# Kernel tuning notes

Hardware: AMD Instinct MI355X
Metric: run time of the kernel (lower is better)

## Reference

```python
import jax, jax.numpy as jnp
import numpy as np

N = 50000
E = 800000
F_IN = 500
H = 5          # heads
C = 32         # per-head channels
HID = H * C    # 160
NC = 20        # num_classes
G = 8          # number of graphs in batch
SLOPE_ATT = 0.2   # GATConv attention leaky slope (PyG default)
SLOPE_ACT = 0.01  # F.leaky_relu default


def _layernorm(x, scale, bias, eps=1e-5):
    mu = jnp.mean(x, axis=-1, keepdims=True)
    var = jnp.var(x, axis=-1, keepdims=True)
    return (x - mu) * jax.lax.rsqrt(var + eps) * scale + bias


def _edge_softmax(logits, dst, num_nodes):
    # segment softmax over incoming edges of each destination node
    m = jax.ops.segment_max(logits, dst, num_segments=num_nodes)
    ex = jnp.exp(logits - m[dst])
    s = jax.ops.segment_sum(ex, dst, num_segments=num_nodes)
    return ex / (s[dst] + 1e-16)


def _gat_layer(x, src, dst, W, a_src, a_dst, b):
    n = x.shape[0]
    h = (x @ W).reshape(n, H, C)                       # [N,H,C]
    al_s = jnp.einsum('nhc,hc->nh', h, a_src)          # [N,H]
    al_d = jnp.einsum('nhc,hc->nh', h, a_dst)
    logits = jax.nn.leaky_relu(al_s[src] + al_d[dst], SLOPE_ATT)  # [Et,H]
    alpha = _edge_softmax(logits, dst, n)              # [Et,H]
    msg = h[src] * alpha[..., None]                    # [Et,H,C]
    out = jax.ops.segment_sum(msg, dst, num_segments=n).reshape(n, HID) + b
    return out, alpha


def setup_inputs():
    key = jax.random.key(0)
    ks = jax.random.split(key, 24)
    p = lambda k, shp: jax.random.normal(k, shp, jnp.float32) * 0.05
    x = jax.random.normal(ks[0], (N, F_IN), jnp.float32)
    edge_index = jax.random.randint(ks[1], (2, E), 0, N, jnp.int64)
    batch = jnp.sort(jax.random.randint(ks[2], (N,), 0, G, jnp.int64))
    return {
        'x': x, 'edge_index': edge_index, 'batch': batch,
        'W1': p(ks[3], (F_IN, HID)), 'a_src1': p(ks[4], (H, C)), 'a_dst1': p(ks[5], (H, C)), 'b1': jnp.zeros((HID,), jnp.float32),
        'ln1_s': jnp.ones((HID,), jnp.float32), 'ln1_b': jnp.zeros((HID,), jnp.float32),
        'W2': p(ks[6], (HID, HID)), 'a_src2': p(ks[7], (H, C)), 'a_dst2': p(ks[8], (H, C)), 'b2': jnp.zeros((HID,), jnp.float32),
        'ln2_s': jnp.ones((HID,), jnp.float32), 'ln2_b': jnp.zeros((HID,), jnp.float32),
        'Wm': p(ks[9], (HID, HID)), 'bm': jnp.zeros((HID,), jnp.float32),
        'Wmlp1': p(ks[10], (HID, HID)), 'bmlp1': jnp.zeros((HID,), jnp.float32),
        'ln3_s': jnp.ones((HID,), jnp.float32), 'ln3_b': jnp.zeros((HID,), jnp.float32),
        'Wmlp2': p(ks[11], (HID, NC)), 'bmlp2': jnp.zeros((NC,), jnp.float32),
    }


def reference(x, edge_index, batch, W1, a_src1, a_dst1, b1, ln1_s, ln1_b,
              W2, a_src2, a_dst2, b2, ln2_s, ln2_b, Wm, bm,
              Wmlp1, bmlp1, ln3_s, ln3_b, Wmlp2, bmlp2):
    n = x.shape[0]
    # PyG GATConv adds self-loops by default
    loops = jnp.arange(n, dtype=edge_index.dtype)
    src = jnp.concatenate([edge_index[0], loops])
    dst = jnp.concatenate([edge_index[1], loops])

    h1, alpha1 = _gat_layer(x, src, dst, W1, a_src1, a_dst1, b1)
    h1 = jax.nn.leaky_relu(h1, SLOPE_ACT)
    h1 = _layernorm(h1, ln1_s, ln1_b)      # dropout = identity at eval

    h2, alpha2 = _gat_layer(h1, src, dst, W2, a_src2, a_dst2, b2)
    h2 = jax.nn.leaky_relu(h2, SLOPE_ACT)
    h2 = _layernorm(h2, ln2_s, ln2_b)

    xo = jax.nn.leaky_relu(h2 @ Wm + bm, SLOPE_ACT)   # [N,HID]

    # global_mean_pool over batch assignment
    sums = jax.ops.segment_sum(xo, batch, num_segments=G)
    cnts = jax.ops.segment_sum(jnp.ones((n, 1), xo.dtype), batch, num_segments=G)
    pooled = sums / jnp.maximum(cnts, 1.0)            # [G,HID]

    z = pooled @ Wmlp1 + bmlp1
    z = jax.nn.relu(_layernorm(z, ln3_s, ln3_b))
    rec = z @ Wmlp2 + bmlp2                           # [G,NC]
    return xo, rec, alpha1, alpha2
```

## Files before the change

kernel.cpp:

```cpp
#include <hip/hip_runtime.h>
#include <hip/hip_bf16.h>
#include <cstdint>
#include <cstddef>

#define NN   50000
#define EE   800000
#define ET_  (EE + NN)
#define FIN  500
#define HID_ 160
#define NC_  20
#define GG   8
#define GB1  ((NN + 63) / 64)
#define NK1  16
#define NK2  5
#define EBH  ((ET_ + 255) / 256)

typedef __attribute__((ext_vector_type(8))) short ab8;
typedef __attribute__((ext_vector_type(4))) float f4;

static __device__ __forceinline__ unsigned short f2bf(float v) {
    union { float f; uint32_t u; } c; c.f = v;
    uint32_t r = c.u + 0x7FFFu + ((c.u >> 16) & 1u);
    return (unsigned short)(r >> 16);
}

static __device__ __forceinline__ float2 bf2f2(uint32_t u) {
    union { uint32_t u; float f; } a, b;
    a.u = u << 16;
    b.u = u & 0xffff0000u;
    return make_float2(a.f, b.f);
}

static __device__ __forceinline__ int lbound_i(const int* arr, int n, int val) {
    int lo = 0, hi = n;
    while (lo < hi) { int mid = (lo + hi) >> 1; if (arr[mid] < val) lo = mid + 1; else hi = mid; }
    return lo;
}

__global__ __launch_bounds__(256) void k_prep0(const float* __restrict__ W1, ab8* __restrict__ B1,
                                               const float* __restrict__ W2, ab8* __restrict__ B2,
                                               const float* __restrict__ Wm, ab8* __restrict__ Bm,
                                               float* __restrict__ pooled, int* __restrict__ deg) {
    int idx = blockIdx.x * 256 + threadIdx.x;
    if (idx < NN) deg[idx] = 0;
    if (idx < GG * HID_) pooled[idx] = 0.f;
    const int C1 = NK1 * 10 * 64;
    const int C2 = NK2 * 10 * 64;
    const float* W; ab8* Bo; int K, cidx;
    if (idx < C1)                { W = W1; Bo = B1; K = FIN;  cidx = idx; }
    else if (idx < C1 + C2)      { W = W2; Bo = B2; K = HID_; cidx = idx - C1; }
    else if (idx < C1 + 2 * C2)  { W = Wm; Bo = Bm; K = HID_; cidx = idx - C1 - C2; }
    else return;
    int s = cidx / 640, r = cidx % 640;
    int t = r >> 6, l = r & 63;
    int fr = l & 15, q = l >> 4;
    int n  = t * 16 + fr;
    int k0 = s * 32 + q * 8;
    unsigned short pk[8];
#pragma unroll
    for (int j = 0; j < 8; j++) {
        int k = k0 + j;
        pk[j] = (k < K) ? f2bf(W[(size_t)k * HID_ + n]) : (unsigned short)0;
    }
    Bo[cidx] = *reinterpret_cast<ab8*>(pk);
}

__global__ __launch_bounds__(256) void k_hist_conv(const int* __restrict__ ei, int* __restrict__ deg,
                                                   const float* __restrict__ x, ab8* __restrict__ Apk) {
    if (blockIdx.x < EBH) {
        int e = blockIdx.x * 256 + threadIdx.x;
        if (e >= ET_) return;
        int d = (e < EE) ? ei[EE + e] : (e - EE);
        atomicAdd(&deg[d], 1);
        return;
    }
    int idx = (blockIdx.x - EBH) * 256 + threadIdx.x;
    int tid = idx & 255;
    int s   = (idx >> 8) & (NK1 - 1);
    int blk = idx >> 12;
    int l = tid & 63, w = tid >> 6;
    int fr = l & 15, q = l >> 4;
    int row = blk * 64 + w * 16 + fr;
    int k0 = s * 32 + q * 8;
    unsigned short pk[8] = {0, 0, 0, 0, 0, 0, 0, 0};
    if (row < NN) {
        const float* xr = &x[(size_t)row * FIN];
        if (k0 + 8 <= FIN) {
            const float4* s4 = reinterpret_cast<const float4*>(&xr[k0]);
            float4 u = s4[0], v = s4[1];
            pk[0] = f2bf(u.x); pk[1] = f2bf(u.y); pk[2] = f2bf(u.z); pk[3] = f2bf(u.w);
            pk[4] = f2bf(v.x); pk[5] = f2bf(v.y); pk[6] = f2bf(v.z); pk[7] = f2bf(v.w);
        } else {
#pragma unroll
            for (int j = 0; j < 8; j++)
                if (k0 + j < FIN) pk[j] = f2bf(xr[k0 + j]);
        }
    }
    Apk[idx] = *reinterpret_cast<ab8*>(pk);
}

__global__ __launch_bounds__(256) void k_scan1(const int* __restrict__ deg, int* __restrict__ rowptr,
                                               int* __restrict__ bsum) {
    __shared__ int s[256];
    int t = threadIdx.x;
    int base = blockIdx.x * 1024 + t * 4;
    int v0 = (base + 0 < NN) ? deg[base + 0] : 0;
    int v1 = (base + 1 < NN) ? deg[base + 1] : 0;
    int v2 = (base + 2 < NN) ? deg[base + 2] : 0;
    int v3 = (base + 3 < NN) ? deg[base + 3] : 0;
    int tot = v0 + v1 + v2 + v3;
    s[t] = tot;
    __syncthreads();
    for (int off = 1; off < 256; off <<= 1) {
        int y = (t >= off) ? s[t - off] : 0;
        __syncthreads();
        s[t] += y;
        __syncthreads();
    }
    int excl = s[t] - tot;
    if (t == 255) bsum[blockIdx.x] = s[255];
    if (base + 0 < NN) rowptr[base + 0] = excl;  excl += v0;
    if (base + 1 < NN) rowptr[base + 1] = excl;  excl += v1;
    if (base + 2 < NN) rowptr[base + 2] = excl;  excl += v2;
    if (base + 3 < NN) rowptr[base + 3] = excl;
}

__global__ void k_scan2(int* __restrict__ bsum, int nb) {
    int t = threadIdx.x;
    int v = (t < nb) ? bsum[t] : 0;
    int orig = v;
    for (int off = 1; off < 64; off <<= 1) {
        int y = __shfl_up(v, off);
        if (t >= off) v += y;
    }
    if (t < nb) bsum[t] = v - orig;
}

__global__ __launch_bounds__(256) void k_scan3(int* __restrict__ rowptr, const int* __restrict__ bsum,
                                               int* __restrict__ cursor) {
    int i = blockIdx.x * 256 + threadIdx.x;
    if (i < NN) {
        int r = rowptr[i] + bsum[i >> 10];
        rowptr[i] = r;
        cursor[i] = r;
    }
    if (i == NN) rowptr[NN] = ET_;
}

__global__ __launch_bounds__(256) void k_scatter(const int* __restrict__ ei, int* __restrict__ cursor,
                                                 int* __restrict__ esrc) {
    int e = blockIdx.x * 256 + threadIdx.x;
    if (e >= ET_) return;
    int s, d;
    if (e < EE) { s = ei[e]; d = ei[EE + e]; } else { s = e - EE; d = e - EE; }
    int slot = atomicAdd(&cursor[d], 1);
    esrc[slot] = s;
}

static __device__ __forceinline__ void gemm_body(int blk,
                                                 const ab8* __restrict__ Apk,
                                                 const ab8* __restrict__ Bpk, int nk,
                                                 float* __restrict__ C, __hip_bfloat16* __restrict__ Cb,
                                                 int M,
                                                 const float* __restrict__ bias, int act,
                                                 const float* __restrict__ asrc, const float* __restrict__ adst,
                                                 float* __restrict__ als_o, float* __restrict__ ald_o,
                                                 const int* __restrict__ batch_p, float* __restrict__ pooled) {
    int tid  = threadIdx.x;
    int lane = tid & 63;
    int w    = tid >> 6;
    int fr   = lane & 15;
    int q    = lane >> 4;
    int row0 = blk * 64;

    f4 acc[10];
#pragma unroll
    for (int t = 0; t < 10; t++) acc[t] = (f4)0.f;

    const ab8* bb  = Bpk + lane;
    const ab8* apk = Apk + (size_t)blk * nk * 256 + tid;

    ab8 bcur[10], bnx[10];
#pragma unroll
    for (int t = 0; t < 10; t++) bcur[t] = bb[t * 64];
    ab8 a0 = apk[0];
    ab8 a1 = apk[256];
    for (int s = 0; s < nk; s++) {
        if (s + 1 < nk) {
#pragma unroll
            for (int t = 0; t < 10; t++) bnx[t] = bb[((s + 1) * 10 + t) * 64];
        }
        ab8 a2 = (ab8)0;
        if (s + 2 < nk) a2 = apk[(s + 2) * 256];
#pragma unroll
        for (int t = 0; t < 10; t++)
            acc[t] = __builtin_amdgcn_mfma_f32_16x16x32_bf16(a0, bcur[t], acc[t], 0, 0, 0);
        a0 = a1; a1 = a2;
#pragma unroll
        for (int t = 0; t < 10; t++) bcur[t] = bnx[t];
    }

    if (als_o) {
        float av_s[10], av_d[10];
#pragma unroll
        for (int t = 0; t < 10; t++) { av_s[t] = asrc[t * 16 + fr]; av_d[t] = adst[t * 16 + fr]; }
#pragma unroll
        for (int i = 0; i < 4; i++) {
            int r = row0 + w * 16 + q * 4 + i;
            float ps[5], pd[5];
#pragma unroll
            for (int h = 0; h < 5; h++) {
                ps[h] = acc[2 * h][i] * av_s[2 * h] + acc[2 * h + 1][i] * av_s[2 * h + 1];
                pd[h] = acc[2 * h][i] * av_d[2 * h] + acc[2 * h + 1][i] * av_d[2 * h + 1];
            }
#pragma unroll
            for (int off = 8; off >= 1; off >>= 1)
#pragma unroll
                for (int h = 0; h < 5; h++) {
                    ps[h] += __shfl_xor(ps[h], off);
                    pd[h] += __shfl_xor(pd[h], off);
                }
            if (fr == 0 && r < M) {
#pragma unroll
                for (int h = 0; h < 5; h++) {
                    als_o[(size_t)r * 8 + h] = ps[h];
                    ald_o[(size_t)r * 8 + h] = pd[h];
                }
            }
        }
    }

    int gu = -2;
    if (pooled) {
        int rhi = row0 + 63; if (rhi >= M) rhi = M - 1;
        int gl = batch_p[row0], gh = batch_p[rhi];
        gu = (gl == gh) ? gl : -1;
    }
    float psum[10];
#pragma unroll
    for (int t = 0; t < 10; t++) psum[t] = 0.f;

    int rbase = row0 + w * 16 + q * 4;
#pragma unroll
    for (int t = 0; t < 10; t++) {
        int col = t * 16 + fr;
        float bv = bias ? bias[col] : 0.f;
#pragma unroll
        for (int i = 0; i < 4; i++) {
            int r = rbase + i;
            float v = acc[t][i] + bv;
            if (act) v = v > 0.f ? v : 0.01f * v;
            if (r < M) {
                if (C)  C[(size_t)r * HID_ + col] = v;
                if (Cb) *reinterpret_cast<unsigned short*>(&Cb[(size_t)r * HID_ + col]) = f2bf(v);
                if (gu >= 0) psum[t] += v;
                else if (gu == -1) atomicAdd(&pooled[batch_p[r] * HID_ + col], v);
            }
        }
    }
    if (gu >= 0) {
#pragma unroll
        for (int t = 0; t < 10; t++) {
            psum[t] += __shfl_xor(psum[t], 16);
            psum[t] += __shfl_xor(psum[t], 32);
        }
        if (q == 0) {
#pragma unroll
            for (int t = 0; t < 10; t++)
                atomicAdd(&pooled[gu * HID_ + t * 16 + fr], psum[t]);
        }
    }
}

__global__ __launch_bounds__(256) void k_gemm_pk(const ab8* __restrict__ Apk,
                                                 const ab8* __restrict__ Bpk, int nk,
                                                 float* __restrict__ C, __hip_bfloat16* __restrict__ Cb,
                                                 int M,
                                                 const float* __restrict__ bias, int act,
                                                 const float* __restrict__ asrc, const float* __restrict__ adst,
                                                 float* __restrict__ als_o, float* __restrict__ ald_o,
                                                 const int* __restrict__ batch_p, float* __restrict__ pooled) {
    gemm_body(blockIdx.x, Apk, Bpk, nk, C, Cb, M, bias, act, asrc, adst, als_o, ald_o, batch_p, pooled);
}

static __device__ __forceinline__ void alpha_body(int e, const int* __restrict__ ei,
                                                  const float* __restrict__ als, const float* __restrict__ ald,
                                                  const float* __restrict__ invb,
                                                  float* __restrict__ alpha_out) {
    if (e >= ET_) return;
    int s, d;
    if (e < EE) { s = ei[e]; d = ei[EE + e]; } else { s = e - EE; d = e - EE; }
    const float* as = &als[(size_t)s * 8];
    float4 a4 = *reinterpret_cast<const float4*>(as);
    float  a5 = as[4];
    float asv[5] = {a4.x, a4.y, a4.z, a4.w, a5};
    const float* adp = &ald[(size_t)d * 8];
    float4 d4 = *reinterpret_cast<const float4*>(adp);
    float  d5 = adp[4];
    float adv[5] = {d4.x, d4.y, d4.z, d4.w, d5};
    const float* ip = &invb[(size_t)d * 8];
    float4 i4 = *reinterpret_cast<const float4*>(ip);
    float  i5 = ip[4];
    float ivv[5] = {i4.x, i4.y, i4.z, i4.w, i5};
    float* ao = &alpha_out[(size_t)e * 5];
#pragma unroll
    for (int h = 0; h < 5; h++) {
        float l = asv[h] + adv[h];
        l = l > 0.f ? l : 0.2f * l;
        float ex = __expf(fminf(l, 60.f));
        ao[h] = ex * ivv[h];
    }
}

__global__ __launch_bounds__(256) void k_gemm_alpha(const ab8* __restrict__ Apk,
                                                    const ab8* __restrict__ Bpk, int nk,
                                                    float* __restrict__ C, __hip_bfloat16* __restrict__ Cb,
                                                    int M,
                                                    const float* __restrict__ bias, int act,
                                                    const float* __restrict__ asrc, const float* __restrict__ adst,
                                                    float* __restrict__ als_o, float* __restrict__ ald_o,
                                                    const int* __restrict__ batch_p, float* __restrict__ pooled,
                                                    const int* __restrict__ ei,
                                                    const float* __restrict__ als_r, const float* __restrict__ ald_r,
                                                    const float* __restrict__ invb, float* __restrict__ alpha_out) {
    if (blockIdx.x < GB1) {
        gemm_body(blockIdx.x, Apk, Bpk, nk, C, Cb, M, bias, act, asrc, adst, als_o, ald_o, batch_p, pooled);
    } else {
        int e = (blockIdx.x - GB1) * 256 + threadIdx.x;
        alpha_body(e, ei, als_r, ald_r, invb, alpha_out);
    }
}

__global__ __launch_bounds__(256) void k_att_agg(const int* __restrict__ rowptr,
                                                 const int* __restrict__ esrc,
                                                 const float* __restrict__ als, const float* __restrict__ ald,
                                                 const __hip_bfloat16* __restrict__ hmat,
                                                 float* __restrict__ alphap,
                                                 float* __restrict__ invb,
                                                 const float* __restrict__ bias,
                                                 const float* __restrict__ lns, const float* __restrict__ lnb,
                                                 uint4* __restrict__ xpk) {
    __shared__ float sExp[4][64 * 5];
    __shared__ int   sSrc[4][64];
    int wv   = threadIdx.x >> 6;
    int lane = threadIdx.x & 63;
    int node = blockIdx.x * 4 + wv;
    if (node >= NN) return;
    int start = rowptr[node], end = rowptr[node + 1];
    int deg = end - start;
    bool fits = (deg <= 64);
    float4 dd4 = *reinterpret_cast<const float4*>(&ald[(size_t)node * 8]);
    float  dd5 = ald[(size_t)node * 8 + 4];
    float ad[5] = {dd4.x, dd4.y, dd4.z, dd4.w, dd5};

    float sm[5] = {0.f, 0.f, 0.f, 0.f, 0.f};
    for (int j = start + lane; j < end; j += 64) {
        int sy = esrc[j];
        int idx = j - start;
        if (fits) sSrc[wv][idx] = sy;
        const float* as = &als[(size_t)sy * 8];
        float4 a4 = *reinterpret_cast<const float4*>(as);
        float  a5 = as[4];
        float asv[5] = {a4.x, a4.y, a4.z, a4.w, a5};
#pragma unroll
        for (int h = 0; h < 5; h++) {
            float l = asv[h] + ad[h];
            l = l > 0.f ? l : 0.2f * l;
            float ex = __expf(fminf(l, 60.f));
            sm[h] += ex;
            if (fits) sExp[wv][idx * 5 + h] = ex;
            else      alphap[(size_t)j * 5 + h] = ex;
        }
    }
#pragma unroll
    for (int off = 32; off >= 1; off >>= 1)
#pragma unroll
        for (int h = 0; h < 5; h++) sm[h] += __shfl_xor(sm[h], off);
    float inv[5];
#pragma unroll
    for (int h = 0; h < 5; h++) inv[h] = 1.f / (sm[h] + 1e-16f);
    if (lane == 0) {
        float* ip = &invb[(size_t)node * 8];
        ip[0] = inv[0]; ip[1] = inv[1]; ip[2] = inv[2]; ip[3] = inv[3]; ip[4] = inv[4];
    }
    if (fits && lane < deg) {
#pragma unroll
        for (int h = 0; h < 5; h++) sExp[wv][lane * 5 + h] *= inv[h];
    }

    int h0 = lane >> 4;
    bool lo16 = lane < 16;
    int c01 = 2 * lane;
    int c2  = 128 + 2 * lane;
    float2 A0 = make_float2(0.f, 0.f), A1 = make_float2(0.f, 0.f);
    float2 A2 = make_float2(0.f, 0.f), A3 = make_float2(0.f, 0.f);
    float2 H0 = make_float2(0.f, 0.f), H1 = make_float2(0.f, 0.f);
    float2 H2 = make_float2(0.f, 0.f), H3 = make_float2(0.f, 0.f);

    if (fits) {
        int idx = 0;
        for (; idx + 3 < deg; idx += 4) {
            int s0 = sSrc[wv][idx], s1 = sSrc[wv][idx + 1];
            int s2 = sSrc[wv][idx + 2], s3 = sSrc[wv][idx + 3];
            float w0 = sExp[wv][(idx + 0) * 5 + h0];
            float w1 = sExp[wv][(idx + 1) * 5 + h0];
            float w2 = sExp[wv][(idx + 2) * 5 + h0];
            float w3 = sExp[wv][(idx + 3) * 5 + h0];
            const unsigned short* r0 = (const unsigned short*)&hmat[(size_t)s0 * HID_];
            const unsigned short* r1 = (const unsigned short*)&hmat[(size_t)s1 * HID_];
            const unsigned short* r2 = (const unsigned short*)&hmat[(size_t)s2 * HID_];
            const unsigned short* r3 = (const unsigned short*)&hmat[(size_t)s3 * HID_];
            float2 f0 = bf2f2(*reinterpret_cast<const uint32_t*>(&r0[c01]));
            float2 f1 = bf2f2(*reinterpret_cast<const uint32_t*>(&r1[c01]));
            float2 f2 = bf2f2(*reinterpret_cast<const uint32_t*>(&r2[c01]));
            float2 f3 = bf2f2(*reinterpret_cast<const uint32_t*>(&r3[c01]));
            A0.x += w0 * f0.x; A0.y += w0 * f0.y;
            A1.x += w1 * f1.x; A1.y += w1 * f1.y;
            A2.x += w2 * f2.x; A2.y += w2 * f2.y;
            A3.x += w3 * f3.x; A3.y += w3 * f3.y;
            if (lo16) {
                float u0 = sExp[wv][(idx + 0) * 5 + 4];
                float u1 = sExp[wv][(idx + 1) * 5 + 4];
                float u2 = sExp[wv][(idx + 2) * 5 + 4];
                float u3 = sExp[wv][(idx + 3) * 5 + 4];
                float2 g0 = bf2f2(*reinterpret_cast<const uint32_t*>(&r0[c2]));
                float2 g1 = bf2f2(*reinterpret_cast<const uint32_t*>(&r1[c2]));
                float2 g2 = bf2f2(*reinterpret_cast<const uint32_t*>(&r2[c2]));
                float2 g3 = bf2f2(*reinterpret_cast<const uint32_t*>(&r3[c2]));
                H0.x += u0 * g0.x; H0.y += u0 * g0.y;
                H1.x += u1 * g1.x; H1.y += u1 * g1.y;
                H2.x += u2 * g2.x; H2.y += u2 * g2.y;
                H3.x += u3 * g3.x; H3.y += u3 * g3.y;
            }
        }
        for (; idx < deg; idx++) {
            int s0 = sSrc[wv][idx];
            float w0 = sExp[wv][idx * 5 + h0];
            const unsigned short* r0 = (const unsigned short*)&hmat[(size_t)s0 * HID_];
            float2 f0 = bf2f2(*reinterpret_cast<const uint32_t*>(&r0[c01]));
            A0.x += w0 * f0.x; A0.y += w0 * f0.y;
            if (lo16) {
                float u0 = sExp[wv][idx * 5 + 4];
                float2 g0 = bf2f2(*reinterpret_cast<const uint32_t*>(&r0[c2]));
                H0.x += u0 * g0.x; H0.y += u0 * g0.y;
            }
        }
    } else {
        for (int j = start; j < end; j++) {
            int s0 = esrc[j];
            float w0 = alphap[(size_t)j * 5 + h0] * inv[h0];
            const unsigned short* r0 = (const unsigned short*)&hmat[(size_t)s0 * HID_];
            float2 f0 = bf2f2(*reinterpret_cast<const uint32_t*>(&r0[c01]));
            A0.x += w0 * f0.x; A0.y += w0 * f0.y;
            if (lo16) {
                float u0 = alphap[(size_t)j * 5 + 4] * inv[4];
                float2 g0 = bf2f2(*reinterpret_cast<const uint32_t*>(&r0[c2]));
                H0.x += u0 * g0.x; H0.y += u0 * g0.y;
            }
        }
    }
    float2 A = make_float2(A0.x + A1.x + A2.x + A3.x, A0.y + A1.y + A2.y + A3.y);
    float2 Hh = make_float2(H0.x + H1.x + H2.x + H3.x, H0.y + H1.y + H2.y + H3.y);

    float2 bb = *reinterpret_cast<const float2*>(&bias[c01]);
    float v0 = A.x + bb.x;  v0 = v0 > 0.f ? v0 : 0.01f * v0;
    float v1 = A.y + bb.y;  v1 = v1 > 0.f ? v1 : 0.01f * v1;
    float v2 = 0.f, v3 = 0.f;
    if (lo16) {
        float2 b2 = *reinterpret_cast<const float2*>(&bias[c2]);
        v2 = Hh.x + b2.x; v2 = v2 > 0.f ? v2 : 0.01f * v2;
        v3 = Hh.y + b2.y; v3 = v3 > 0.f ? v3 : 0.01f * v3;
    }
    float s  = v0 + v1 + v2 + v3;
    float sq = v0 * v0 + v1 * v1 + v2 * v2 + v3 * v3;
#pragma unroll
    for (int off = 32; off >= 1; off >>= 1) {
        s  += __shfl_xor(s, off);
        sq += __shfl_xor(sq, off);
    }
    float m = s * (1.f / 160.f);
    float r = rsqrtf(sq * (1.f / 160.f) - m * m + 1e-5f);
    uint32_t pk1, pk2 = 0u;
    {
        float2 sc = *reinterpret_cast<const float2*>(&lns[c01]);
        float2 bi = *reinterpret_cast<const float2*>(&lnb[c01]);
        pk1 = (uint32_t)f2bf((v0 - m) * r * sc.x + bi.x)
            | ((uint32_t)f2bf((v1 - m) * r * sc.y + bi.y) << 16);
    }
    if (lo16) {
        float2 sc = *reinterpret_cast<const float2*>(&lns[c2]);
        float2 bi = *reinterpret_cast<const float2*>(&lnb[c2]);
        pk2 = (uint32_t)f2bf((v2 - m) * r * sc.x + bi.x)
            | ((uint32_t)f2bf((v3 - m) * r * sc.y + bi.y) << 16);
    }
    int j = lane;
    int srcb = (j < 16) ? (4 * j) : (4 * ((j - 16) & 15));
    uint32_t a0w = __shfl(pk1, srcb + 0), a1w = __shfl(pk1, srcb + 1);
    uint32_t a2w = __shfl(pk1, srcb + 2), a3w = __shfl(pk1, srcb + 3);
    uint32_t b0w = __shfl(pk2, srcb + 0), b1w = __shfl(pk2, srcb + 1);
    uint32_t b2w = __shfl(pk2, srcb + 2), b3w = __shfl(pk2, srcb + 3);
    if (j < 20) {
        uint4 val;
        val.x = (j < 16) ? a0w : b0w;
        val.y = (j < 16) ? a1w : b1w;
        val.z = (j < 16) ? a2w : b2w;
        val.w = (j < 16) ? a3w : b3w;
        int blk = node >> 6, wq = (node >> 4) & 3, fr = node & 15;
        int ks = j >> 2, q = j & 3;
        size_t cidx = (size_t)(blk * NK2 + ks) * 256 + wq * 64 + q * 16 + fr;
        xpk[cidx] = val;
    }
}

__global__ __launch_bounds__(256) void k_mlp(const float* __restrict__ pooled, const int* __restrict__ batch,
                                             const float* __restrict__ W1, const float* __restrict__ b1,
                                             const float* __restrict__ lns, const float* __restrict__ lnb,
                                             const float* __restrict__ W2, const float* __restrict__ b2,
                                             float* __restrict__ rec) {
    __shared__ float P[GG][HID_];
    __shared__ float Z[GG][HID_];
    __shared__ float mu[GG], rr[GG], ic[GG];
    int t = threadIdx.x;
    if (t < GG) {
        int lo = lbound_i(batch, NN, t), hi = lbound_i(batch, NN, t + 1);
        ic[t] = 1.f / fmaxf((float)(hi - lo), 1.f);
    }
    __syncthreads();
    for (int i = t; i < GG * HID_; i += 256) P[i / HID_][i % HID_] = pooled[i] * ic[i / HID_];
    __syncthreads();
    for (int i = t; i < GG * HID_; i += 256) {
        int g = i / HID_, j = i % HID_;
        float acc = b1[j];
        for (int k = 0; k < HID_; k++) acc += P[g][k] * W1[k * HID_ + j];
        Z[g][j] = acc;
    }
    __syncthreads();
    if (t < GG) {
        float s = 0.f, sq = 0.f;
        for (int k = 0; k < HID_; k++) { float z = Z[t][k]; s += z; sq += z * z; }
        float m = s / (float)HID_;
        mu[t] = m;
        rr[t] = rsqrtf(sq / (float)HID_ - m * m + 1e-5f);
    }
    __syncthreads();
    for (int i = t; i < GG * HID_; i += 256) {
        int g = i / HID_, j = i % HID_;
        float z = (Z[g][j] - mu[g]) * rr[g] * lns[j] + lnb[j];
        Z[g][j] = fmaxf(z, 0.f);
    }
    __syncthreads();
    for (int i = t; i < GG * NC_; i += 256) {
        int g = i / NC_, j = i % NC_;
        float acc = b2[j];
        for (int k = 0; k < HID_; k++) acc += Z[g][k] * W2[k * NC_ + j];
        rec[g * NC_ + j] = acc;
    }
}

extern "C" void kernel_launch(void* const* d_in, const int* in_sizes, int n_in,
                              void* d_out, int out_size, void* d_ws, size_t ws_size,
                              hipStream_t stream) {
    const float* x    = (const float*)d_in[0];
    const int*   ei   = (const int*)d_in[1];
    const int*   batch= (const int*)d_in[2];
    const float* W1   = (const float*)d_in[3];
    const float* as1  = (const float*)d_in[4];
    const float* ad1  = (const float*)d_in[5];
    const float* b1   = (const float*)d_in[6];
    const float* ln1s = (const float*)d_in[7];
    const float* ln1b = (const float*)d_in[8];
    const float* W2   = (const float*)d_in[9];
    const float* as2  = (const float*)d_in[10];
    const float* ad2  = (const float*)d_in[11];
    const float* b2   = (const float*)d_in[12];
    const float* ln2s = (const float*)d_in[13];
    const float* ln2b = (const float*)d_in[14];
    const float* Wm   = (const float*)d_in[15];
    const float* bm   = (const float*)d_in[16];
    const float* Wm1  = (const float*)d_in[17];
    const float* bm1  = (const float*)d_in[18];
    const float* ln3s = (const float*)d_in[19];
    const float* ln3b = (const float*)d_in[20];
    const float* Wm2  = (const float*)d_in[21];
    const float* bm2  = (const float*)d_in[22];

    float* out    = (float*)d_out;
    float* xo     = out;
    float* rec    = out + (size_t)NN * HID_;
    float* alpha1 = rec + GG * NC_;
    float* alpha2 = alpha1 + (size_t)ET_ * 5;

    char* w = (char*)d_ws;
    auto carve = [&](size_t bytes) { char* p = w; w += (bytes + 255) & ~(size_t)255; return p; };
    int*   deg    = (int*)carve((size_t)NN * 4);
    int*   rowptr = (int*)carve((size_t)(NN + 1) * 4);
    int*   cursor = (int*)carve((size_t)NN * 4);
    int*   esrc   = (int*)carve((size_t)ET_ * 4);
    int*   bsum   = (int*)carve(64 * 4);
    __hip_bfloat16* hbuf = (__hip_bfloat16*)carve((size_t)NN * HID_ * 2);
    uint4* xpk    = (uint4*)carve((size_t)GB1 * NK2 * 256 * 16);
    float* alphap = (float*)carve((size_t)ET_ * 5 * 4);
    float* als1   = (float*)carve((size_t)NN * 8 * 4);
    float* ald1   = (float*)carve((size_t)NN * 8 * 4);
    float* als2   = (float*)carve((size_t)NN * 8 * 4);
    float* ald2   = (float*)carve((size_t)NN * 8 * 4);
    float* invb   = (float*)carve((size_t)NN * 8 * 4);
    float* pooled = (float*)carve((size_t)GG * HID_ * 4);
    ab8*   B1pk   = (ab8*)carve((size_t)NK1 * 10 * 64 * 16);
    ab8*   B2pk   = (ab8*)carve((size_t)NK2 * 10 * 64 * 16);
    ab8*   Bmpk   = (ab8*)carve((size_t)NK2 * 10 * 64 * 16);
    ab8*   Apk    = (ab8*)d_out;

    k_prep0<<<(NN + 255) / 256, 256, 0, stream>>>(W1, B1pk, W2, B2pk, Wm, Bmpk, pooled, deg);

    k_hist_conv<<<EBH + GB1 * NK1, 256, 0, stream>>>(ei, deg, x, Apk);

    int nb = (NN + 1023) / 1024;
    k_scan1<<<nb, 256, 0, stream>>>(deg, rowptr, bsum);
    k_scan2<<<1, 64, 0, stream>>>(bsum, nb);
    k_scan3<<<(NN + 1 + 255) / 256, 256, 0, stream>>>(rowptr, bsum, cursor);
    k_scatter<<<EBH, 256, 0, stream>>>(ei, cursor, esrc);

    const int NWB = (NN + 3) / 4;

    k_gemm_pk<<<GB1, 256, 0, stream>>>(Apk, B1pk, NK1, nullptr, hbuf, NN, nullptr, 0,
                                       as1, ad1, als1, ald1, nullptr, nullptr);
    k_att_agg<<<NWB, 256, 0, stream>>>(rowptr, esrc, als1, ald1, hbuf, alphap, invb,
                                       b1, ln1s, ln1b, xpk);

    k_gemm_alpha<<<GB1 + EBH, 256, 0, stream>>>((const ab8*)xpk, B2pk, NK2, nullptr, hbuf, NN,
                                                nullptr, 0, as2, ad2, als2, ald2, nullptr, nullptr,
                                                ei, als1, ald1, invb, alpha1);

    k_att_agg<<<NWB, 256, 0, stream>>>(rowptr, esrc, als2, ald2, hbuf, alphap, invb,
                                       b2, ln2s, ln2b, xpk);

    k_gemm_alpha<<<GB1 + EBH, 256, 0, stream>>>((const ab8*)xpk, Bmpk, NK2, xo, nullptr, NN,
                                                bm, 1, nullptr, nullptr, nullptr, nullptr, batch, pooled,
                                                ei, als2, ald2, invb, alpha2);

    k_mlp<<<1, 256, 0, stream>>>(pooled, batch, Wm1, bm1, ln3s, ln3b, Wm2, bm2, rec);
}
```

Baseline: 612.2 us.

## Coalesce x bf16 packing via LDS transpose and fuse edge scatter into GEMM1

The x-to-bf16 packing path now has one block per 64 rows. Each block reads whole rows with coalesced float4 loads, transposes them through a swizzled LDS buffer into the MFMA fragment layout, and writes contiguous packed output. Before, each thread gathered 8 strided floats. The CSR edge scatter kernel is merged into the first GEMM launch as extra blocks, which removes one launch and lets the atomic scatter overlap the GEMM. In exchange, the conversion blocks use 32KB of LDS and three barriers per half, which may reduce occupancy.

```diff
diff --git a/kernel.cpp b/kernel.cpp
--- a/kernel.cpp
+++ b/kernel.cpp
@@ -67,36 +67,48 @@
 
 __global__ __launch_bounds__(256) void k_hist_conv(const int* __restrict__ ei, int* __restrict__ deg,
                                                    const float* __restrict__ x, ab8* __restrict__ Apk) {
-    if (blockIdx.x < EBH) {
-        int e = blockIdx.x * 256 + threadIdx.x;
+    if (blockIdx.x >= GB1) {
+        int e = (blockIdx.x - GB1) * 256 + threadIdx.x;
         if (e >= ET_) return;
         int d = (e < EE) ? ei[EE + e] : (e - EE);
         atomicAdd(&deg[d], 1);
         return;
     }
-    int idx = (blockIdx.x - EBH) * 256 + threadIdx.x;
-    int tid = idx & 255;
-    int s   = (idx >> 8) & (NK1 - 1);
-    int blk = idx >> 12;
-    int l = tid & 63, w = tid >> 6;
-    int fr = l & 15, q = l >> 4;
-    int row = blk * 64 + w * 16 + fr;
-    int k0 = s * 32 + q * 8;
-    unsigned short pk[8] = {0, 0, 0, 0, 0, 0, 0, 0};
-    if (row < NN) {
-        const float* xr = &x[(size_t)row * FIN];
-        if (k0 + 8 <= FIN) {
-            const float4* s4 = reinterpret_cast<const float4*>(&xr[k0]);
-            float4 u = s4[0], v = s4[1];
-            pk[0] = f2bf(u.x); pk[1] = f2bf(u.y); pk[2] = f2bf(u.z); pk[3] = f2bf(u.w);
-            pk[4] = f2bf(v.x); pk[5] = f2bf(v.y); pk[6] = f2bf(v.z); pk[7] = f2bf(v.w);
-        } else {
-#pragma unroll
-            for (int j = 0; j < 8; j++)
-                if (k0 + j < FIN) pk[j] = f2bf(xr[k0 + j]);
-        }
-    }
-    Apk[idx] = *reinterpret_cast<ab8*>(pk);
+    __shared__ uint2 lds2[4096];
+    int blk = blockIdx.x;
+    int tid = threadIdx.x;
+    const float4* xf4 = (const float4*)x;
+    uint4* ap4 = (uint4*)Apk;
+#pragma unroll
+    for (int h = 0; h < 2; h++) {
+        for (int i = tid; i < 4096; i += 256) lds2[i] = make_uint2(0u, 0u);
+        __syncthreads();
+        int rbase = blk * 64 + h * 32;
+        for (int i = tid; i < 4000; i += 256) {
+            int rl = i / 125, j = i - rl * 125;
+            int g = rbase + rl;
+            if (g < NN) {
+                float4 v = xf4[(size_t)g * 125 + j];
+                uint32_t lo = (uint32_t)f2bf(v.x) | ((uint32_t)f2bf(v.y) << 16);
+                uint32_t hi = (uint32_t)f2bf(v.z) | ((uint32_t)f2bf(v.w) << 16);
+                int k = j * 4;
+                int s = k >> 5, q = (k >> 3) & 3, e2 = (k & 7) >> 2;
+                int woff = rl >> 4, fr = rl & 15;
+                int idx = s * 128 + woff * 64 + q * 16 + fr;
+                int p = idx ^ (((s << 2) | q) & 7);
+                lds2[2 * p + e2] = make_uint2(lo, hi);
+            }
+        }
+        __syncthreads();
+        for (int i = tid; i < 2048; i += 256) {
+            int s = i >> 7, off = i & 127;
+            int q = (off >> 4) & 3;
+            int p = i ^ (((s << 2) | q) & 7);
+            uint2 a = lds2[2 * p], b = lds2[2 * p + 1];
+            ap4[(size_t)(blk * NK1 + s) * 256 + h * 128 + off] = make_uint4(a.x, a.y, b.x, b.y);
+        }
+        __syncthreads();
+    }
 }
 
 __global__ __launch_bounds__(256) void k_scan1(const int* __restrict__ deg, int* __restrict__ rowptr,
@@ -147,16 +159,6 @@
     if (i == NN) rowptr[NN] = ET_;
 }
 
-__global__ __launch_bounds__(256) void k_scatter(const int* __restrict__ ei, int* __restrict__ cursor,
-                                                 int* __restrict__ esrc) {
-    int e = blockIdx.x * 256 + threadIdx.x;
-    if (e >= ET_) return;
-    int s, d;
-    if (e < EE) { s = ei[e]; d = ei[EE + e]; } else { s = e - EE; d = e - EE; }
-    int slot = atomicAdd(&cursor[d], 1);
-    esrc[slot] = s;
-}
-
 static __device__ __forceinline__ void gemm_body(int blk,
                                                  const ab8* __restrict__ Apk,
                                                  const ab8* __restrict__ Bpk, int nk,
@@ -272,15 +274,26 @@
     }
 }
 
-__global__ __launch_bounds__(256) void k_gemm_pk(const ab8* __restrict__ Apk,
-                                                 const ab8* __restrict__ Bpk, int nk,
-                                                 float* __restrict__ C, __hip_bfloat16* __restrict__ Cb,
-                                                 int M,
-                                                 const float* __restrict__ bias, int act,
-                                                 const float* __restrict__ asrc, const float* __restrict__ adst,
-                                                 float* __restrict__ als_o, float* __restrict__ ald_o,
-                                                 const int* __restrict__ batch_p, float* __restrict__ pooled) {
-    gemm_body(blockIdx.x, Apk, Bpk, nk, C, Cb, M, bias, act, asrc, adst, als_o, ald_o, batch_p, pooled);
+__global__ __launch_bounds__(256) void k_gemm_scatter(const ab8* __restrict__ Apk,
+                                                      const ab8* __restrict__ Bpk, int nk,
+                                                      float* __restrict__ C, __hip_bfloat16* __restrict__ Cb,
+                                                      int M,
+                                                      const float* __restrict__ bias, int act,
+                                                      const float* __restrict__ asrc, const float* __restrict__ adst,
+                                                      float* __restrict__ als_o, float* __restrict__ ald_o,
+                                                      const int* __restrict__ batch_p, float* __restrict__ pooled,
+                                                      const int* __restrict__ ei, int* __restrict__ cursor,
+                                                      int* __restrict__ esrc) {
+    if (blockIdx.x < GB1) {
+        gemm_body(blockIdx.x, Apk, Bpk, nk, C, Cb, M, bias, act, asrc, adst, als_o, ald_o, batch_p, pooled);
+    } else {
+        int e = (blockIdx.x - GB1) * 256 + threadIdx.x;
+        if (e >= ET_) return;
+        int s, d;
+        if (e < EE) { s = ei[e]; d = ei[EE + e]; } else { s = e - EE; d = e - EE; }
+        int slot = atomicAdd(&cursor[d], 1);
+        esrc[slot] = s;
+    }
 }
 
 static __device__ __forceinline__ void alpha_body(int e, const int* __restrict__ ei,
@@ -613,18 +626,19 @@
 
     k_prep0<<<(NN + 255) / 256, 256, 0, stream>>>(W1, B1pk, W2, B2pk, Wm, Bmpk, pooled, deg);
 
-    k_hist_conv<<<EBH + GB1 * NK1, 256, 0, stream>>>(ei, deg, x, Apk);
+    k_hist_conv<<<GB1 + EBH, 256, 0, stream>>>(ei, deg, x, Apk);
 
     int nb = (NN + 1023) / 1024;
     k_scan1<<<nb, 256, 0, stream>>>(deg, rowptr, bsum);
     k_scan2<<<1, 64, 0, stream>>>(bsum, nb);
     k_scan3<<<(NN + 1 + 255) / 256, 256, 0, stream>>>(rowptr, bsum, cursor);
-    k_scatter<<<EBH, 256, 0, stream>>>(ei, cursor, esrc);
 
     const int NWB = (NN + 3) / 4;
 
-    k_gemm_pk<<<GB1, 256, 0, stream>>>(Apk, B1pk, NK1, nullptr, hbuf, NN, nullptr, 0,
-                                       as1, ad1, als1, ald1, nullptr, nullptr);
+    k_gemm_scatter<<<GB1 + EBH, 256, 0, stream>>>(Apk, B1pk, NK1, nullptr, hbuf, NN, nullptr, 0,
+                                                  as1, ad1, als1, ald1, nullptr, nullptr,
+                                                  ei, cursor, esrc);
+
     k_att_agg<<<NWB, 256, 0, stream>>>(rowptr, esrc, als1, ald1, hbuf, alphap, invb,
                                        b1, ln1s, ln1b, xpk);
 
```

Measured after the change: 600.2 us. -2.0%, faster.
